# Optimization experiments

Measured on AMD Instinct MI355X. Metric: run time of the kernel, lower is better.

The kernel has to match this reference:

```python
import jax, jax.numpy as jnp
import numpy as np

V, E, C = 50000, 5000, 16
TAU = 0.5
EPS = 1e-08
SPARSITY = 0.02  # fraction of (v,e) incidences


def setup_inputs() -> dict:
    key = jax.random.key(0)
    k1, k2, k3, k4 = jax.random.split(key, 4)
    pred_s = jax.random.normal(k1, (V, C), dtype=jnp.float32)
    pred_t = jax.random.normal(k2, (V, C), dtype=jnp.float32)
    # binary incidence matrix; pin vertex 0 into every edge so deg_e > 0
    H = (jax.random.uniform(k3, (V, E)) < SPARSITY).astype(jnp.float32)
    H = H.at[0, :].set(1.0)
    e_mask = jax.random.randint(k4, (E,), 0, 2).astype(jnp.bool_)
    return {"pred_s": pred_s, "pred_t": pred_t, "H": H, "e_mask": e_mask}


def _v2e_mean(p, H, deg_e):
    # == einsum('vc,ve->ec', p, H @ diag(1/deg_e)) : column-normalized scatter-mean
    return jnp.einsum('ve,vc->ec', H, p) / deg_e[:, None]


def reference(pred_s, pred_t, H, e_mask):
    ps = jax.nn.softmax(pred_s, axis=1)   # [V, C]
    pt = jax.nn.softmax(pred_t, axis=1)   # [V, C]
    deg_e = H.sum(axis=0)                 # [E]
    log_s = jnp.log(_v2e_mean(ps, H, deg_e) / TAU + EPS)  # [E, C]
    log_t = jnp.log(_v2e_mean(pt, H, deg_e) / TAU + EPS)  # [E, C]
    # F.kl_div(input=log_s, target=log_t, log_target=True, reduction='batchmean')
    # restricted to masked edges; mask via weights to keep shapes static.
    kl = jnp.exp(log_t) * (log_t - log_s)                  # [E, C]
    m = e_mask.astype(kl.dtype)                            # [E]
    n_sel = jnp.maximum(m.sum(), 1.0)
    return (kl * m[:, None]).sum() / n_sel
```

## Files before the change

### kernel.cpp

```cpp
#include <hip/hip_runtime.h>

#define NV 50000
#define NE 5000
#define NC 16
#define TAU_INV 2.0f
#define EPS 1e-8f

#define NCH 100
#define VCH 500
#define GRP 2
#define NXB 5
#define NBLK (NXB * NCH)
#define NLANE 5120

typedef float vf4 __attribute__((ext_vector_type(4)));

__global__ __launch_bounds__(256) void softmax_kernel(
    const float* __restrict__ pred_s, const float* __restrict__ pred_t,
    float* __restrict__ p) {
  int i = blockIdx.x * 256 + threadIdx.x;
  if (i >= 2 * NV) return;
  const float* src;
  float* dst;
  if (i < NV) { src = pred_s + (size_t)i * NC; dst = p + (size_t)i * 32; }
  else        { int j = i - NV; src = pred_t + (size_t)j * NC; dst = p + (size_t)j * 32 + 16; }
  float4 a = ((const float4*)src)[0];
  float4 b = ((const float4*)src)[1];
  float4 c = ((const float4*)src)[2];
  float4 d = ((const float4*)src)[3];
  float x[16] = {a.x,a.y,a.z,a.w, b.x,b.y,b.z,b.w, c.x,c.y,c.z,c.w, d.x,d.y,d.z,d.w};
  float mx = x[0];
#pragma unroll
  for (int k = 1; k < 16; ++k) mx = fmaxf(mx, x[k]);
  float sum = 0.f;
#pragma unroll
  for (int k = 0; k < 16; ++k) { x[k] = expf(x[k] - mx); sum += x[k]; }
  float inv = 1.f / sum;
#pragma unroll
  for (int k = 0; k < 16; ++k) x[k] *= inv;
  float4 o0 = {x[0], x[1], x[2], x[3]};
  float4 o1 = {x[4], x[5], x[6], x[7]};
  float4 o2 = {x[8], x[9], x[10], x[11]};
  float4 o3 = {x[12], x[13], x[14], x[15]};
  ((float4*)dst)[0] = o0;
  ((float4*)dst)[1] = o1;
  ((float4*)dst)[2] = o2;
  ((float4*)dst)[3] = o3;
}

__global__ __launch_bounds__(256) void accum_kernel(
    const float* __restrict__ H, const float* __restrict__ p,
    float* __restrict__ part) {
  __shared__ float lp[VCH * 32];
  int b = blockIdx.x;
  int item;
  if (b < 496) item = (b & 7) * 62 + (b >> 3);
  else         item = b;
  int xb = item % NXB;
  int y  = item / NXB;
  int e0 = 4 * (xb * 256 + (int)threadIdx.x);
  if (e0 > NE - 4) e0 = NE - 4;
  int v0 = y * VCH;

  {
    const float4* __restrict__ src = (const float4*)(p + (size_t)v0 * 32);
    float4* dst = (float4*)lp;
    for (int i = threadIdx.x; i < VCH * 8; i += 256) dst[i] = src[i];
  }
  __syncthreads();

  float4 aS[16], aT[16], dg;
#pragma unroll
  for (int k = 0; k < 16; ++k) {
    aS[k] = make_float4(0.f, 0.f, 0.f, 0.f);
    aT[k] = make_float4(0.f, 0.f, 0.f, 0.f);
  }
  dg = make_float4(0.f, 0.f, 0.f, 0.f);

  const float* __restrict__ hp = H + (size_t)v0 * NE + e0;

  vf4 hc[GRP];
#pragma unroll
  for (int u = 0; u < GRP; ++u)
    hc[u] = __builtin_nontemporal_load((const vf4*)(hp + (size_t)u * NE));

  for (int vb = 0; vb < VCH; vb += GRP) {
    int nb = (vb + GRP < VCH) ? vb + GRP : vb;
    vf4 hn[GRP];
#pragma unroll
    for (int u = 0; u < GRP; ++u)
      hn[u] = __builtin_nontemporal_load((const vf4*)(hp + (size_t)(nb + u) * NE));

#pragma unroll
    for (int u = 0; u < GRP; ++u) {
      const float4* __restrict__ r = (const float4*)(lp + (size_t)(vb + u) * 32);
      vf4 h = hc[u];
      dg.x += h.x; dg.y += h.y; dg.z += h.z; dg.w += h.w;
      {
        float4 s0 = r[0], s1 = r[1], s2 = r[2], s3 = r[3];
        float sv[16] = {s0.x,s0.y,s0.z,s0.w, s1.x,s1.y,s1.z,s1.w,
                        s2.x,s2.y,s2.z,s2.w, s3.x,s3.y,s3.z,s3.w};
#pragma unroll
        for (int k = 0; k < 16; ++k) {
          aS[k].x = fmaf(h.x, sv[k], aS[k].x);
          aS[k].y = fmaf(h.y, sv[k], aS[k].y);
          aS[k].z = fmaf(h.z, sv[k], aS[k].z);
          aS[k].w = fmaf(h.w, sv[k], aS[k].w);
        }
      }
      {
        float4 t0 = r[4], t1 = r[5], t2 = r[6], t3 = r[7];
        float tv[16] = {t0.x,t0.y,t0.z,t0.w, t1.x,t1.y,t1.z,t1.w,
                        t2.x,t2.y,t2.z,t2.w, t3.x,t3.y,t3.z,t3.w};
#pragma unroll
        for (int k = 0; k < 16; ++k) {
          aT[k].x = fmaf(h.x, tv[k], aT[k].x);
          aT[k].y = fmaf(h.y, tv[k], aT[k].y);
          aT[k].z = fmaf(h.z, tv[k], aT[k].z);
          aT[k].w = fmaf(h.w, tv[k], aT[k].w);
        }
      }
    }
#pragma unroll
    for (int u = 0; u < GRP; ++u) hc[u] = hn[u];
  }

  float* op = part + (size_t)y * 33 * NLANE + e0;
#pragma unroll
  for (int k = 0; k < 16; ++k) {
    vf4 w = {aS[k].x, aS[k].y, aS[k].z, aS[k].w};
    __builtin_nontemporal_store(w, (vf4*)(op + (size_t)k * NLANE));
  }
#pragma unroll
  for (int k = 0; k < 16; ++k) {
    vf4 w = {aT[k].x, aT[k].y, aT[k].z, aT[k].w};
    __builtin_nontemporal_store(w, (vf4*)(op + (size_t)(16 + k) * NLANE));
  }
  {
    vf4 w = {dg.x, dg.y, dg.z, dg.w};
    __builtin_nontemporal_store(w, (vf4*)(op + (size_t)32 * NLANE));
  }
}

__global__ __launch_bounds__(256) void reduce_kernel(
    const float* __restrict__ part, float* __restrict__ acc) {
  int i = blockIdx.x * 256 + threadIdx.x;
  if (i >= 33 * NLANE) return;
  float s = 0.f;
#pragma unroll 4
  for (int y = 0; y < NCH; ++y)
    s += __builtin_nontemporal_load(part + (size_t)y * 33 * NLANE + i);
  acc[i] = s;
}

__global__ __launch_bounds__(256) void kl_kernel(
    const float* __restrict__ acc, const unsigned char* __restrict__ e_mask,
    float* __restrict__ out) {
  __shared__ float snum[4];
  __shared__ float scnt[4];
  int t = threadIdx.x;
  float num = 0.f, cnt = 0.f;
  for (int e = t; e < NE; e += 256) {
    if (e_mask[e]) {
      float deg = acc[(size_t)32 * NLANE + e];
      float invd = 1.f / deg;
      float kl = 0.f;
#pragma unroll
      for (int k = 0; k < 16; ++k) {
        float ms = acc[(size_t)k * NLANE + e] * invd;
        float mt = acc[(size_t)(16 + k) * NLANE + e] * invd;
        float xs = ms * TAU_INV + EPS;
        float xt = mt * TAU_INV + EPS;
        kl += xt * (logf(xt) - logf(xs));
      }
      num += kl;
      cnt += 1.f;
    }
  }
#pragma unroll
  for (int off = 32; off > 0; off >>= 1) {
    num += __shfl_down(num, off, 64);
    cnt += __shfl_down(cnt, off, 64);
  }
  if ((t & 63) == 0) { snum[t >> 6] = num; scnt[t >> 6] = cnt; }
  __syncthreads();
  if (t == 0) {
    float n = snum[0] + snum[1] + snum[2] + snum[3];
    float c2 = scnt[0] + scnt[1] + scnt[2] + scnt[3];
    out[0] = n / fmaxf(c2, 1.f);
  }
}

extern "C" void kernel_launch(void* const* d_in, const int* in_sizes, int n_in,
                              void* d_out, int out_size, void* d_ws, size_t ws_size,
                              hipStream_t stream) {
  const float* pred_s = (const float*)d_in[0];
  const float* pred_t = (const float*)d_in[1];
  const float* H      = (const float*)d_in[2];
  const unsigned char* e_mask = (const unsigned char*)d_in[3];

  float* ws   = (float*)d_ws;
  float* p    = ws;
  float* acc  = ws + (size_t)NV * 32;
  float* part = acc + (size_t)33 * NLANE;

  softmax_kernel<<<dim3((2 * NV + 255) / 256), 256, 0, stream>>>(pred_s, pred_t, p);
  accum_kernel<<<dim3(NBLK), 256, 0, stream>>>(H, p, part);
  reduce_kernel<<<dim3((33 * NLANE + 255) / 256), 256, 0, stream>>>(part, acc);
  kl_kernel<<<1, 256, 0, stream>>>(acc, e_mask, (float*)d_out);
}
```

Measured before the change: 1.346 ms.

## Halve per-thread edge width, stage LDS in halves, vectorize partial reduction

Each accumulate thread now covers 2 edges instead of 4, which halves the accumulator registers and doubles the number of blocks. LDS staging is split into two 250-vertex stages, and launch bounds request 4 blocks per CU to raise occupancy and hide latency on the streaming H reads. The block-index swizzle is rewritten for 1000 blocks, and the reduce kernel now loads float4 vectors. In exchange, each LDS row read is reused across half as many edges, so LDS traffic per FMA doubles, and each thread issues narrower H loads.

```diff
diff --git a/kernel.cpp b/kernel.cpp
--- a/kernel.cpp
+++ b/kernel.cpp
@@ -8,12 +8,15 @@
 
 #define NCH 100
 #define VCH 500
-#define GRP 2
-#define NXB 5
+#define VST 250
+#define GRP 5
+#define EPL 2
+#define NXB 10
 #define NBLK (NXB * NCH)
 #define NLANE 5120
 
 typedef float vf4 __attribute__((ext_vector_type(4)));
+typedef float vf2 __attribute__((ext_vector_type(2)));
 
 __global__ __launch_bounds__(256) void softmax_kernel(
     const float* __restrict__ pred_s, const float* __restrict__ pred_t,
@@ -48,109 +51,107 @@
   ((float4*)dst)[3] = o3;
 }
 
-__global__ __launch_bounds__(256) void accum_kernel(
+#define FMA4(ACC, B, Q) \
+  ACC[B+0].x = fmaf(h.x, Q.x, ACC[B+0].x); ACC[B+0].y = fmaf(h.y, Q.x, ACC[B+0].y); \
+  ACC[B+1].x = fmaf(h.x, Q.y, ACC[B+1].x); ACC[B+1].y = fmaf(h.y, Q.y, ACC[B+1].y); \
+  ACC[B+2].x = fmaf(h.x, Q.z, ACC[B+2].x); ACC[B+2].y = fmaf(h.y, Q.z, ACC[B+2].y); \
+  ACC[B+3].x = fmaf(h.x, Q.w, ACC[B+3].x); ACC[B+3].y = fmaf(h.y, Q.w, ACC[B+3].y);
+
+__global__ __launch_bounds__(256, 4) void accum_kernel(
     const float* __restrict__ H, const float* __restrict__ p,
     float* __restrict__ part) {
-  __shared__ float lp[VCH * 32];
+  __shared__ float lp[VST * 32];
   int b = blockIdx.x;
-  int item;
-  if (b < 496) item = (b & 7) * 62 + (b >> 3);
-  else         item = b;
+  int item = (b & 7) * 125 + (b >> 3);
   int xb = item % NXB;
   int y  = item / NXB;
-  int e0 = 4 * (xb * 256 + (int)threadIdx.x);
-  if (e0 > NE - 4) e0 = NE - 4;
+  int e0 = EPL * (xb * 256 + (int)threadIdx.x);
+  if (e0 > NE - EPL) e0 = NE - EPL;
   int v0 = y * VCH;
 
+  float2 aS[16], aT[16];
+#pragma unroll
+  for (int k = 0; k < 16; ++k) {
+    aS[k] = make_float2(0.f, 0.f);
+    aT[k] = make_float2(0.f, 0.f);
+  }
+  float2 dg = make_float2(0.f, 0.f);
+
+  const float* __restrict__ hp_base = H + (size_t)v0 * NE + e0;
+
+  for (int st = 0; st < 2; ++st) {
+    __syncthreads();
+    {
+      const float4* __restrict__ src =
+          (const float4*)(p + (size_t)(v0 + st * VST) * 32);
+      float4* dst = (float4*)lp;
+      for (int i = threadIdx.x; i < VST * 8; i += 256) dst[i] = src[i];
+    }
+    __syncthreads();
+
+    const float* __restrict__ hp = hp_base + (size_t)(st * VST) * NE;
+
+    vf2 hc[GRP];
+#pragma unroll
+    for (int u = 0; u < GRP; ++u)
+      hc[u] = __builtin_nontemporal_load((const vf2*)(hp + (size_t)u * NE));
+
+    for (int vb = 0; vb < VST; vb += GRP) {
+      int nb = (vb + GRP < VST) ? vb + GRP : vb;
+      vf2 hn[GRP];
+#pragma unroll
+      for (int u = 0; u < GRP; ++u)
+        hn[u] = __builtin_nontemporal_load((const vf2*)(hp + (size_t)(nb + u) * NE));
+
+#pragma unroll
+      for (int u = 0; u < GRP; ++u) {
+        const float4* __restrict__ r = (const float4*)(lp + (size_t)(vb + u) * 32);
+        vf2 h = hc[u];
+        dg.x += h.x; dg.y += h.y;
+        float4 q;
+        q = r[0]; FMA4(aS, 0, q)
+        q = r[1]; FMA4(aS, 4, q)
+        q = r[2]; FMA4(aS, 8, q)
+        q = r[3]; FMA4(aS, 12, q)
+        q = r[4]; FMA4(aT, 0, q)
+        q = r[5]; FMA4(aT, 4, q)
+        q = r[6]; FMA4(aT, 8, q)
+        q = r[7]; FMA4(aT, 12, q)
+      }
+#pragma unroll
+      for (int u = 0; u < GRP; ++u) hc[u] = hn[u];
+    }
+  }
+
+  float* op = part + (size_t)y * 33 * NLANE + e0;
+#pragma unroll
+  for (int k = 0; k < 16; ++k) {
+    vf2 w = {aS[k].x, aS[k].y};
+    __builtin_nontemporal_store(w, (vf2*)(op + (size_t)k * NLANE));
+  }
+#pragma unroll
+  for (int k = 0; k < 16; ++k) {
+    vf2 w = {aT[k].x, aT[k].y};
+    __builtin_nontemporal_store(w, (vf2*)(op + (size_t)(16 + k) * NLANE));
+  }
   {
-    const float4* __restrict__ src = (const float4*)(p + (size_t)v0 * 32);
-    float4* dst = (float4*)lp;
-    for (int i = threadIdx.x; i < VCH * 8; i += 256) dst[i] = src[i];
-  }
-  __syncthreads();
-
-  float4 aS[16], aT[16], dg;
-#pragma unroll
-  for (int k = 0; k < 16; ++k) {
-    aS[k] = make_float4(0.f, 0.f, 0.f, 0.f);
-    aT[k] = make_float4(0.f, 0.f, 0.f, 0.f);
-  }
-  dg = make_float4(0.f, 0.f, 0.f, 0.f);
-
-  const float* __restrict__ hp = H + (size_t)v0 * NE + e0;
-
-  vf4 hc[GRP];
-#pragma unroll
-  for (int u = 0; u < GRP; ++u)
-    hc[u] = __builtin_nontemporal_load((const vf4*)(hp + (size_t)u * NE));
-
-  for (int vb = 0; vb < VCH; vb += GRP) {
-    int nb = (vb + GRP < VCH) ? vb + GRP : vb;
-    vf4 hn[GRP];
-#pragma unroll
-    for (int u = 0; u < GRP; ++u)
-      hn[u] = __builtin_nontemporal_load((const vf4*)(hp + (size_t)(nb + u) * NE));
-
-#pragma unroll
-    for (int u = 0; u < GRP; ++u) {
-      const float4* __restrict__ r = (const float4*)(lp + (size_t)(vb + u) * 32);
-      vf4 h = hc[u];
-      dg.x += h.x; dg.y += h.y; dg.z += h.z; dg.w += h.w;
-      {
-        float4 s0 = r[0], s1 = r[1], s2 = r[2], s3 = r[3];
-        float sv[16] = {s0.x,s0.y,s0.z,s0.w, s1.x,s1.y,s1.z,s1.w,
-                        s2.x,s2.y,s2.z,s2.w, s3.x,s3.y,s3.z,s3.w};
-#pragma unroll
-        for (int k = 0; k < 16; ++k) {
-          aS[k].x = fmaf(h.x, sv[k], aS[k].x);
-          aS[k].y = fmaf(h.y, sv[k], aS[k].y);
-          aS[k].z = fmaf(h.z, sv[k], aS[k].z);
-          aS[k].w = fmaf(h.w, sv[k], aS[k].w);
-        }
-      }
-      {
-        float4 t0 = r[4], t1 = r[5], t2 = r[6], t3 = r[7];
-        float tv[16] = {t0.x,t0.y,t0.z,t0.w, t1.x,t1.y,t1.z,t1.w,
-                        t2.x,t2.y,t2.z,t2.w, t3.x,t3.y,t3.z,t3.w};
-#pragma unroll
-        for (int k = 0; k < 16; ++k) {
-          aT[k].x = fmaf(h.x, tv[k], aT[k].x);
-          aT[k].y = fmaf(h.y, tv[k], aT[k].y);
-          aT[k].z = fmaf(h.z, tv[k], aT[k].z);
-          aT[k].w = fmaf(h.w, tv[k], aT[k].w);
-        }
-      }
-    }
-#pragma unroll
-    for (int u = 0; u < GRP; ++u) hc[u] = hn[u];
-  }
-
-  float* op = part + (size_t)y * 33 * NLANE + e0;
-#pragma unroll
-  for (int k = 0; k < 16; ++k) {
-    vf4 w = {aS[k].x, aS[k].y, aS[k].z, aS[k].w};
-    __builtin_nontemporal_store(w, (vf4*)(op + (size_t)k * NLANE));
-  }
-#pragma unroll
-  for (int k = 0; k < 16; ++k) {
-    vf4 w = {aT[k].x, aT[k].y, aT[k].z, aT[k].w};
-    __builtin_nontemporal_store(w, (vf4*)(op + (size_t)(16 + k) * NLANE));
-  }
-  {
-    vf4 w = {dg.x, dg.y, dg.z, dg.w};
-    __builtin_nontemporal_store(w, (vf4*)(op + (size_t)32 * NLANE));
+    vf2 w = {dg.x, dg.y};
+    __builtin_nontemporal_store(w, (vf2*)(op + (size_t)32 * NLANE));
   }
 }
 
 __global__ __launch_bounds__(256) void reduce_kernel(
     const float* __restrict__ part, float* __restrict__ acc) {
   int i = blockIdx.x * 256 + threadIdx.x;
-  if (i >= 33 * NLANE) return;
-  float s = 0.f;
+  if (i >= 33 * NLANE / 4) return;
+  vf4 s = {0.f, 0.f, 0.f, 0.f};
+  const vf4* __restrict__ pp = (const vf4*)part;
 #pragma unroll 4
-  for (int y = 0; y < NCH; ++y)
-    s += __builtin_nontemporal_load(part + (size_t)y * 33 * NLANE + i);
-  acc[i] = s;
+  for (int y = 0; y < NCH; ++y) {
+    vf4 v = __builtin_nontemporal_load(pp + (size_t)y * (33 * NLANE / 4) + i);
+    s.x += v.x; s.y += v.y; s.z += v.z; s.w += v.w;
+  }
+  ((vf4*)acc)[i] = s;
 }
 
 __global__ __launch_bounds__(256) void kl_kernel(
@@ -206,6 +207,6 @@
 
   softmax_kernel<<<dim3((2 * NV + 255) / 256), 256, 0, stream>>>(pred_s, pred_t, p);
   accum_kernel<<<dim3(NBLK), 256, 0, stream>>>(H, p, part);
-  reduce_kernel<<<dim3((33 * NLANE + 255) / 256), 256, 0, stream>>>(part, acc);
+  reduce_kernel<<<dim3((33 * NLANE / 4 + 255) / 256), 256, 0, stream>>>(part, acc);
   kl_kernel<<<1, 256, 0, stream>>>(acc, e_mask, (float*)d_out);
 }
```

Result: slower. 2.033 ms (+51.1%).
